# Optimization experiments

Measured on AMD Instinct MI355X. Metric: run time of the kernel, lower is better.

## Reference

```python
import jax, jax.numpy as jnp
from jax import lax
import numpy as np

B, H, W = 4, 2048, 2048
FG_DENSITY = 0.1  # below 8-connectivity percolation threshold -> small components


def setup_inputs() -> dict:
    key = jax.random.key(0)
    # binary foreground mask, as the torch module expects (x == 1 selects pixels)
    x = (jax.random.uniform(key, (B, H, W)) < FG_DENSITY).astype(jnp.float32)
    return {"x": x}


def _pool3x3(m):
    # torch.nn.MaxPool2d(kernel=3, stride=1, padding=1); -inf padding matches
    # torch's max-pool padding semantics (all labels are >= 0 anyway).
    return lax.reduce_window(m, -jnp.inf, lax.max,
                             window_dimensions=(1, 3, 3),
                             window_strides=(1, 1, 1),
                             padding=((0, 0), (1, 1), (1, 1)))


def reference(x):
    b, h, w = x.shape
    mult = h * w
    # per-pixel initial labels: mult - linear_index, reshaped to [H, W]
    weights = (jnp.float32(mult) - jnp.arange(mult, dtype=jnp.float32)).reshape(h, w)
    sel = x == 1.0                      # foreground selector (constant)
    mask0 = x * weights                 # background pixels get label 0

    # Iterate max-pool label propagation to the fixed point. The torch loop
    # stops when torch.unique count stabilizes; since the update is monotone
    # non-decreasing and bounded, that is exactly the fixed point reached here.
    def cond(state):
        _, converged = state
        return jnp.logical_not(converged)

    def body(state):
        m, _ = state
        new = jnp.where(sel, _pool3x3(m), m)
        return new, jnp.all(new == m)

    mask, _ = lax.while_loop(cond, body, (mask0, jnp.array(False)))
    return mask
```

## Files before the change

kernel.cpp:

```cpp
#include <hip/hip_runtime.h>


constexpr int W_DIM = 2048;
constexpr int H_DIM = 2048;
constexpr int MULT  = W_DIM * H_DIM;
constexpr int TILE  = 64;
constexpr int TPX   = TILE * TILE;
constexpr int BLK   = 256;
constexpr int TILES_PER_IMG = MULT / TPX;
constexpr int NB    = (H_DIM / TILE) - 1;
constexpr int WCAP  = 512;
constexpr int OVF_CAP = 65536;

__device__ __forceinline__ int find_root(const int* p, int v) {
    int q = p[v];
    while (q != v) { v = q; q = p[v]; }
    return v;
}

__device__ __forceinline__ void merge_uf(int* p, int a, int b) {
    while (true) {
        a = find_root(p, a);
        b = find_root(p, b);
        if (a == b) return;
        if (a < b) { int t = a; a = b; b = t; }
        int old = atomicMin(&p[a], b);
        if (old == a) return;
        a = old;
    }
}

template <int MODE>
__global__ __launch_bounds__(BLK) void cc_local(const float* __restrict__ x,
                                                int* __restrict__ parent,
                                                float* __restrict__ out,
                                                unsigned long long* __restrict__ bitmap,
                                                int2* __restrict__ slabs,
                                                int* __restrict__ wl_cnt,
                                                int2* __restrict__ ovf,
                                                int* __restrict__ ovf_cnt) {
    __shared__ int lp[TPX];
    __shared__ unsigned long long rowmask_sh[TILE];
    __shared__ unsigned int bc[TPX / 32];
    __shared__ int cursor;

    const int t    = threadIdx.x;
    const int wave = t >> 6;
    const int lane = t & 63;
    const int tile = blockIdx.x;
    const int img  = tile / TILES_PER_IMG;
    const int tl   = tile % TILES_PER_IMG;
    const int tr   = tl >> 5;
    const int tc   = tl & 31;
    const int origin = img * MULT + (tr * TILE) * W_DIM + tc * TILE;

    unsigned long long m[16];
    #pragma unroll
    for (int rr = 0; rr < 16; ++rr) {
        int row = wave * 16 + rr;
        float v = x[origin + row * W_DIM + lane];
        m[rr] = __ballot(v != 0.0f);
    }
    if (lane == 0) {
        #pragma unroll
        for (int rr = 0; rr < 16; ++rr) {
            rowmask_sh[wave * 16 + rr] = m[rr];
            if constexpr (MODE == 1) {
                int grow = tr * TILE + wave * 16 + rr;
                bitmap[(img * H_DIM + grow) * (W_DIM / 64) + tc] = m[rr];
            }
        }
    }
    if constexpr (MODE == 1) {
        if (t < TPX / 32) bc[t] = 0u;
        if (t == 0) cursor = 0;
    }
    #pragma unroll
    for (int j = 0; j < 4; ++j) {
        int s = t + BLK * j;
        int b = s * 4;
        reinterpret_cast<int4*>(lp)[s] = make_int4(b, b + 1, b + 2, b + 3);
    }
    __syncthreads();

    const unsigned long long mu0 = (wave > 0) ? rowmask_sh[wave * 16 - 1] : 0ULL;

    unsigned long long bits = 0ULL;
    #pragma unroll
    for (int rr = 0; rr < 16; ++rr) {
        const unsigned long long mm = m[rr];
        const unsigned long long mu = (rr == 0) ? mu0 : m[rr - 1];
        const unsigned long long lmask  = mm & (mm << 1);
        const unsigned long long bfmask = mm & mu & ~((mm << 1) & (mu << 1));
        const unsigned long long afmask = mm & (mu << 1) & ~mu & ~(mm << 1);
        const unsigned long long cfmask = mm & (mu >> 1) & ~mu;
        unsigned nib = (unsigned)((lmask  >> lane) & 1ULL)
                     | ((unsigned)((bfmask >> lane) & 1ULL) << 1)
                     | ((unsigned)((afmask >> lane) & 1ULL) << 2)
                     | ((unsigned)((cfmask >> lane) & 1ULL) << 3);
        bits |= (unsigned long long)nib << (rr * 4);
    }

    while (__any(bits != 0ULL)) {
        if (bits) {
            int idx = (int)__builtin_ctzll(bits);
            bits &= bits - 1;
            int rr = idx >> 2, ty = idx & 3;
            int p  = (wave * 16 + rr) * TILE + lane;
            int off = (ty & 2) ? ((ty & 1) ? -(TILE - 1) : -(TILE + 1))
                               : ((ty & 1) ? -TILE : -1);
            merge_uf(lp, p, p + off);
        }
    }
    __syncthreads();

    if constexpr (MODE == 1) {
        int p = -1;
        bool mark = false;
        if      (wave == 0) { if (tr > 0)  { p = lane;                      mark = (rowmask_sh[0]    >> lane) & 1ULL; } }
        else if (wave == 3) { if (tr < 31) { p = (TILE - 1) * TILE + lane;  mark = (rowmask_sh[63]   >> lane) & 1ULL; } }
        else if (wave == 1) { if (tc > 0)  { p = lane * TILE;               mark = rowmask_sh[lane] & 1ULL; } }
        else                { if (tc < 31) { p = lane * TILE + (TILE - 1);  mark = (rowmask_sh[lane] >> 63) & 1ULL; } }
        if (mark) {
            int v = find_root(lp, p);
            atomicOr(&bc[v >> 5], 1u << (v & 31));
            int rg = origin + (v >> 6) * W_DIM + (v & (TILE - 1));
            int pg = origin + (p >> 6) * W_DIM + (p & (TILE - 1));
            parent[pg] = rg;
        }
        __syncthreads();
    }

    unsigned ndbits = 0;
    #pragma unroll
    for (int j = 0; j < 4; ++j) {
        int s   = t + BLK * j;
        int row = s >> 4;
        int c4  = s & 15;
        int p0  = row * TILE + c4 * 4;
        int4 q  = reinterpret_cast<const int4*>(lp)[s];
        unsigned fgbits = (unsigned)((rowmask_sh[row] >> (c4 * 4)) & 0xFULL);
        int vr[4];
        {
            int v = q.x, p = p0;
            if ((fgbits & 1u) && v != p) { int w = lp[v]; while (w != v) { v = w; w = lp[v]; } }
            vr[0] = v;
        }
        {
            int v = q.y, p = p0 + 1;
            if ((fgbits & 2u) && v != p) { int w = lp[v]; while (w != v) { v = w; w = lp[v]; } }
            vr[1] = v;
        }
        {
            int v = q.z, p = p0 + 2;
            if ((fgbits & 4u) && v != p) { int w = lp[v]; while (w != v) { v = w; w = lp[v]; } }
            vr[2] = v;
        }
        {
            int v = q.w, p = p0 + 3;
            if ((fgbits & 8u) && v != p) { int w = lp[v]; while (w != v) { v = w; w = lp[v]; } }
            vr[3] = v;
        }

        if constexpr (MODE == 0) {
            int4 o;
            o.x = (fgbits & 1u) ? origin + (vr[0] >> 6) * W_DIM + (vr[0] & (TILE - 1)) : -1;
            o.y = (fgbits & 2u) ? origin + (vr[1] >> 6) * W_DIM + (vr[1] & (TILE - 1)) : -1;
            o.z = (fgbits & 4u) ? origin + (vr[2] >> 6) * W_DIM + (vr[2] & (TILE - 1)) : -1;
            o.w = (fgbits & 8u) ? origin + (vr[3] >> 6) * W_DIM + (vr[3] & (TILE - 1)) : -1;
            reinterpret_cast<int4*>(parent + origin + row * W_DIM)[c4] = o;
        } else {
            float4 o;
            float lab[4];
            #pragma unroll
            for (int k = 0; k < 4; ++k) {
                int v = vr[k];
                bool fg = (fgbits >> k) & 1u;
                int g = origin + (v >> 6) * W_DIM + (v & (TILE - 1));
                lab[k] = fg ? (float)(MULT - (g & (MULT - 1))) : 0.0f;
                bool nd = fg && ((bc[v >> 5] >> (v & 31)) & 1u);
                if (nd) {
                    ndbits |= 1u << (j * 4 + k);
                    if (v == p0 + k) parent[g] = g;
                }
            }
            o.x = lab[0]; o.y = lab[1]; o.z = lab[2]; o.w = lab[3];
            reinterpret_cast<float4*>(out + origin + row * W_DIM)[c4] = o;
        }
    }

    if constexpr (MODE == 1) {
        if (ndbits) {
            int cnt  = __popc(ndbits);
            int base = atomicAdd(&cursor, cnt);
            while (ndbits) {
                int b = (int)__builtin_ctz(ndbits);
                ndbits &= ndbits - 1;
                int j = b >> 2, k = b & 3;
                int s   = t + BLK * j;
                int row = s >> 4;
                int c4  = s & 15;
                int p   = row * TILE + c4 * 4 + k;
                int v   = find_root(lp, p);
                int g   = origin + (v >> 6) * W_DIM + (v & (TILE - 1));
                int pg  = origin + row * W_DIM + c4 * 4 + k;
                int off = base++;
                if (off < WCAP) slabs[tile * WCAP + off] = make_int2(pg, g);
                else {
                    int oi = atomicAdd(ovf_cnt, 1);
                    if (oi < OVF_CAP) ovf[oi] = make_int2(pg, g);
                }
            }
        }
        __syncthreads();
        if (t == 0) wl_cnt[tile] = (cursor < WCAP) ? cursor : WCAP;
    }
}

__global__ void cc_zero(int* p) { *p = 0; }

__global__ __launch_bounds__(BLK) void cc_border_bm(const unsigned long long* __restrict__ bm,
                                                    int* __restrict__ parent, int total) {
    int tid = blockIdx.x * blockDim.x + threadIdx.x;
    if (tid >= total) return;
    const int per_img = 2 * NB * W_DIM;
    int img = tid / per_img;
    int k   = tid % per_img;
    int base = img * MULT;
    const unsigned long long* b = bm + (size_t)img * H_DIM * (W_DIM / 64);
    auto FG = [&](int r, int c) -> bool {
        return (b[r * (W_DIM / 64) + (c >> 6)] >> (c & 63)) & 1ULL;
    };
    if (k < NB * W_DIM) {
        int r = TILE * (1 + k / W_DIM);
        int c = k % W_DIM;
        if (!FG(r, c)) return;
        int i  = base + r * W_DIM + c;
        int up = i - W_DIM;
        if (FG(r - 1, c))                    merge_uf(parent, i, up);
        if (c > 0         && FG(r - 1, c - 1)) merge_uf(parent, i, up - 1);
        if (c < W_DIM - 1 && FG(r - 1, c + 1)) merge_uf(parent, i, up + 1);
    } else {
        int m2 = k - NB * W_DIM;
        int c = TILE * (1 + m2 / H_DIM);
        int r = m2 % H_DIM;
        if (!FG(r, c)) return;
        int i   = base + r * W_DIM + c;
        int lft = i - 1;
        if (FG(r, c - 1))                      merge_uf(parent, i, lft);
        if (r > 0         && FG(r - 1, c - 1)) merge_uf(parent, i, lft - W_DIM);
        if (r < H_DIM - 1 && FG(r + 1, c - 1)) merge_uf(parent, i, lft + W_DIM);
    }
}

__global__ __launch_bounds__(BLK) void cc_fixup(const int2* __restrict__ slabs,
                                                const int* __restrict__ wl_cnt,
                                                const int2* __restrict__ ovf,
                                                const int* __restrict__ ovf_cnt,
                                                const int* __restrict__ parent,
                                                float* __restrict__ out, int ntiles) {
    int tid = blockIdx.x * blockDim.x + threadIdx.x;
    int slab_total = ntiles * WCAP;
    int2 e;
    if (tid < slab_total) {
        int tile = tid / WCAP, slot = tid - tile * WCAP;
        if (slot >= wl_cnt[tile]) return;
        e = slabs[tid];
    } else {
        int oi = tid - slab_total;
        int oc = *ovf_cnt; if (oc > OVF_CAP) oc = OVF_CAP;
        if (oi >= oc) return;
        e = ovf[oi];
    }
    int root = find_root(parent, e.y);
    out[e.x] = (float)(MULT - (root & (MULT - 1)));
}

__global__ __launch_bounds__(BLK) void cc_border(int* __restrict__ parent, int total) {
    int tid = blockIdx.x * blockDim.x + threadIdx.x;
    if (tid >= total) return;
    const int per_img = 2 * NB * W_DIM;
    int img = tid / per_img;
    int k   = tid % per_img;
    int base = img * MULT;
    if (k < NB * W_DIM) {
        int r = TILE * (1 + k / W_DIM);
        int c = k % W_DIM;
        int i = base + r * W_DIM + c;
        if (parent[i] < 0) return;
        int up = i - W_DIM;
        if (parent[up] >= 0)                      merge_uf(parent, i, up);
        if (c > 0         && parent[up - 1] >= 0) merge_uf(parent, i, up - 1);
        if (c < W_DIM - 1 && parent[up + 1] >= 0) merge_uf(parent, i, up + 1);
    } else {
        int m2 = k - NB * W_DIM;
        int c = TILE * (1 + m2 / H_DIM);
        int r = m2 % H_DIM;
        int i = base + r * W_DIM + c;
        if (parent[i] < 0) return;
        int lft = i - 1;
        if (parent[lft] >= 0)                            merge_uf(parent, i, lft);
        if (r > 0         && parent[lft - W_DIM] >= 0)   merge_uf(parent, i, lft - W_DIM);
        if (r < H_DIM - 1 && parent[lft + W_DIM] >= 0)   merge_uf(parent, i, lft + W_DIM);
    }
}

__global__ __launch_bounds__(BLK) void cc_write(const int* __restrict__ parent,
                                                float* __restrict__ out, int n4) {
    int i = blockIdx.x * blockDim.x + threadIdx.x;
    if (i >= n4) return;
    int4 p = reinterpret_cast<const int4*>(parent)[i];
    int a0 = (p.x >= 0) ? parent[p.x] : 0;
    int a1 = (p.y >= 0) ? parent[p.y] : 0;
    int a2 = (p.z >= 0) ? parent[p.z] : 0;
    int a3 = (p.w >= 0) ? parent[p.w] : 0;
    float4 o;
    { int v = p.x, w = a0; if (v >= 0) { while (w != v) { v = w; w = parent[v]; } }
      o.x = (p.x < 0) ? 0.f : (float)(MULT - (v & (MULT - 1))); }
    { int v = p.y, w = a1; if (v >= 0) { while (w != v) { v = w; w = parent[v]; } }
      o.y = (p.y < 0) ? 0.f : (float)(MULT - (v & (MULT - 1))); }
    { int v = p.z, w = a2; if (v >= 0) { while (w != v) { v = w; w = parent[v]; } }
      o.z = (p.z < 0) ? 0.f : (float)(MULT - (v & (MULT - 1))); }
    { int v = p.w, w = a3; if (v >= 0) { while (w != v) { v = w; w = parent[v]; } }
      o.w = (p.w < 0) ? 0.f : (float)(MULT - (v & (MULT - 1))); }
    reinterpret_cast<float4*>(out)[i] = o;
}

__global__ __launch_bounds__(BLK) void cc_flatten(int* __restrict__ parent, int n) {
    int i = blockIdx.x * blockDim.x + threadIdx.x;
    if (i >= n) return;
    int p = parent[i];
    if (p < 0 || p == i) return;
    int r = find_root(parent, p);
    if (r != p) parent[i] = r;
}

__global__ __launch_bounds__(BLK) void cc_final_inplace(int* __restrict__ parent, int n4) {
    int i = blockIdx.x * blockDim.x + threadIdx.x;
    if (i >= n4) return;
    int4 p = reinterpret_cast<const int4*>(parent)[i];
    float4 o;
    o.x = (p.x < 0) ? 0.f : (float)(MULT - (p.x & (MULT - 1)));
    o.y = (p.y < 0) ? 0.f : (float)(MULT - (p.y & (MULT - 1)));
    o.z = (p.z < 0) ? 0.f : (float)(MULT - (p.z & (MULT - 1)));
    o.w = (p.w < 0) ? 0.f : (float)(MULT - (p.w & (MULT - 1)));
    reinterpret_cast<float4*>(parent)[i] = o;
}

extern "C" void kernel_launch(void* const* d_in, const int* in_sizes, int n_in,
                              void* d_out, int out_size, void* d_ws, size_t ws_size,
                              hipStream_t stream) {
    const float* x = (const float*)d_in[0];
    const int n     = in_sizes[0];
    const int n_img = n / MULT;
    const int n4    = n / 4;
    const int tiles = n_img * TILES_PER_IMG;
    const int border_threads = n_img * 2 * NB * W_DIM;

    size_t off_parent = 0;
    size_t off_bitmap = off_parent + (size_t)n * 4;
    size_t off_slabs  = off_bitmap + (size_t)n / 8;
    size_t off_cnt    = off_slabs  + (size_t)tiles * WCAP * 8;
    size_t off_ovf    = off_cnt    + (size_t)tiles * 4;
    size_t off_ovfcnt = off_ovf    + (size_t)OVF_CAP * 8;
    size_t need_fused = off_ovfcnt + 128;

    dim3 blk(BLK);
    if (ws_size >= need_fused) {
        char* ws = (char*)d_ws;
        int*  parent  = (int*)(ws + off_parent);
        unsigned long long* bitmap = (unsigned long long*)(ws + off_bitmap);
        int2* slabs   = (int2*)(ws + off_slabs);
        int*  wl_cnt  = (int*)(ws + off_cnt);
        int2* ovf     = (int2*)(ws + off_ovf);
        int*  ovf_cnt = (int*)(ws + off_ovfcnt);
        float* out    = (float*)d_out;

        cc_zero<<<1, 1, 0, stream>>>(ovf_cnt);
        cc_local<1><<<tiles, blk, 0, stream>>>(x, parent, out, bitmap,
                                               slabs, wl_cnt, ovf, ovf_cnt);
        cc_border_bm<<<(border_threads + BLK - 1) / BLK, blk, 0, stream>>>(bitmap, parent, border_threads);
        int fix_threads = tiles * WCAP + OVF_CAP;
        cc_fixup<<<(fix_threads + BLK - 1) / BLK, blk, 0, stream>>>(slabs, wl_cnt, ovf, ovf_cnt,
                                                                    parent, out, tiles);
    } else {
        const bool use_ws = (ws_size >= (size_t)n * sizeof(int));
        int* parent = use_ws ? (int*)d_ws : (int*)d_out;
        cc_local<0><<<tiles, blk, 0, stream>>>(x, parent, nullptr, nullptr,
                                               nullptr, nullptr, nullptr, nullptr);
        cc_border<<<(border_threads + BLK - 1) / BLK, blk, 0, stream>>>(parent, border_threads);
        if (use_ws) {
            cc_write<<<(n4 + BLK - 1) / BLK, blk, 0, stream>>>(parent, (float*)d_out, n4);
        } else {
            cc_flatten      <<<(n + BLK - 1) / BLK, blk, 0, stream>>>(parent, n);
            cc_final_inplace<<<(n4 + BLK - 1) / BLK, blk, 0, stream>>>(parent, n4);
        }
    }
}
```

Measured before the change: 64.04 us.

## Pack border-root flag into local parent array and enqueue worklist inline

Stores the 'touches tile border' flag as a high bit in the shared union-find parent array instead of a separate bitmap, so the final root walk yields both root and flag. Worklist entries are appended inline with per-element shared atomics instead of a second find_root pass. Root self-parent writes move to the border-marking step. The fixup kernel skips writes when the root did not change, and the zeroing kernel is replaced by a memset. The trade-off is more contended shared-memory atomics on the cursor and an extra mask in every find step.

```diff
diff --git a/kernel.cpp b/kernel.cpp
--- a/kernel.cpp
+++ b/kernel.cpp
@@ -11,10 +11,18 @@
 constexpr int NB    = (H_DIM / TILE) - 1;
 constexpr int WCAP  = 512;
 constexpr int OVF_CAP = 65536;
+constexpr int PMASK = 0xFFFF;
+constexpr int BFLAG = 0x10000;
 
 __device__ __forceinline__ int find_root(const int* p, int v) {
     int q = p[v];
     while (q != v) { v = q; q = p[v]; }
+    return v;
+}
+
+__device__ __forceinline__ int find_root_m(const int* p, int v) {
+    int q = p[v] & PMASK;
+    while (q != v) { v = q; q = p[v] & PMASK; }
     return v;
 }
 
@@ -41,7 +49,6 @@
                                                 int* __restrict__ ovf_cnt) {
     __shared__ int lp[TPX];
     __shared__ unsigned long long rowmask_sh[TILE];
-    __shared__ unsigned int bc[TPX / 32];
     __shared__ int cursor;
 
     const int t    = threadIdx.x;
@@ -52,7 +59,9 @@
     const int tl   = tile % TILES_PER_IMG;
     const int tr   = tl >> 5;
     const int tc   = tl & 31;
-    const int origin = img * MULT + (tr * TILE) * W_DIM + tc * TILE;
+    const int origin    = img * MULT + (tr * TILE) * W_DIM + tc * TILE;
+    const int img_base  = img * MULT;
+    const int base_loc  = origin - img_base;
 
     unsigned long long m[16];
     #pragma unroll
@@ -72,7 +81,6 @@
         }
     }
     if constexpr (MODE == 1) {
-        if (t < TPX / 32) bc[t] = 0u;
         if (t == 0) cursor = 0;
     }
     #pragma unroll
@@ -122,44 +130,60 @@
         else if (wave == 1) { if (tc > 0)  { p = lane * TILE;               mark = rowmask_sh[lane] & 1ULL; } }
         else                { if (tc < 31) { p = lane * TILE + (TILE - 1);  mark = (rowmask_sh[lane] >> 63) & 1ULL; } }
         if (mark) {
-            int v = find_root(lp, p);
-            atomicOr(&bc[v >> 5], 1u << (v & 31));
+            int v = find_root_m(lp, p);
+            atomicOr(&lp[v], BFLAG);
             int rg = origin + (v >> 6) * W_DIM + (v & (TILE - 1));
             int pg = origin + (p >> 6) * W_DIM + (p & (TILE - 1));
             parent[pg] = rg;
+            parent[rg] = rg;
         }
         __syncthreads();
     }
 
-    unsigned ndbits = 0;
     #pragma unroll
     for (int j = 0; j < 4; ++j) {
         int s   = t + BLK * j;
         int row = s >> 4;
         int c4  = s & 15;
         int p0  = row * TILE + c4 * 4;
-        int4 q  = reinterpret_cast<const int4*>(lp)[s];
+        int4 qv = reinterpret_cast<const int4*>(lp)[s];
         unsigned fgbits = (unsigned)((rowmask_sh[row] >> (c4 * 4)) & 0xFULL);
-        int vr[4];
+        int vr[4], qf[4];
         {
-            int v = q.x, p = p0;
-            if ((fgbits & 1u) && v != p) { int w = lp[v]; while (w != v) { v = w; w = lp[v]; } }
-            vr[0] = v;
+            int q = qv.x, v = q & PMASK, p = p0;
+            if ((fgbits & 1u) && v != p) {
+                int w = lp[v];
+                while ((w & PMASK) != v) { v = w & PMASK; w = lp[v]; }
+                q = w;
+            }
+            vr[0] = v; qf[0] = q;
         }
         {
-            int v = q.y, p = p0 + 1;
-            if ((fgbits & 2u) && v != p) { int w = lp[v]; while (w != v) { v = w; w = lp[v]; } }
-            vr[1] = v;
+            int q = qv.y, v = q & PMASK, p = p0 + 1;
+            if ((fgbits & 2u) && v != p) {
+                int w = lp[v];
+                while ((w & PMASK) != v) { v = w & PMASK; w = lp[v]; }
+                q = w;
+            }
+            vr[1] = v; qf[1] = q;
         }
         {
-            int v = q.z, p = p0 + 2;
-            if ((fgbits & 4u) && v != p) { int w = lp[v]; while (w != v) { v = w; w = lp[v]; } }
-            vr[2] = v;
+            int q = qv.z, v = q & PMASK, p = p0 + 2;
+            if ((fgbits & 4u) && v != p) {
+                int w = lp[v];
+                while ((w & PMASK) != v) { v = w & PMASK; w = lp[v]; }
+                q = w;
+            }
+            vr[2] = v; qf[2] = q;
         }
         {
-            int v = q.w, p = p0 + 3;
-            if ((fgbits & 8u) && v != p) { int w = lp[v]; while (w != v) { v = w; w = lp[v]; } }
-            vr[3] = v;
+            int q = qv.w, v = q & PMASK, p = p0 + 3;
+            if ((fgbits & 8u) && v != p) {
+                int w = lp[v];
+                while ((w & PMASK) != v) { v = w & PMASK; w = lp[v]; }
+                q = w;
+            }
+            vr[3] = v; qf[3] = q;
         }
 
         if constexpr (MODE == 0) {
@@ -170,54 +194,34 @@
             o.w = (fgbits & 8u) ? origin + (vr[3] >> 6) * W_DIM + (vr[3] & (TILE - 1)) : -1;
             reinterpret_cast<int4*>(parent + origin + row * W_DIM)[c4] = o;
         } else {
-            float4 o;
             float lab[4];
             #pragma unroll
             for (int k = 0; k < 4; ++k) {
-                int v = vr[k];
+                int v  = vr[k];
                 bool fg = (fgbits >> k) & 1u;
-                int g = origin + (v >> 6) * W_DIM + (v & (TILE - 1));
-                lab[k] = fg ? (float)(MULT - (g & (MULT - 1))) : 0.0f;
-                bool nd = fg && ((bc[v >> 5] >> (v & 31)) & 1u);
-                if (nd) {
-                    ndbits |= 1u << (j * 4 + k);
-                    if (v == p0 + k) parent[g] = g;
+                int rl = base_loc + ((v >> 6) << 11) + (v & (TILE - 1));
+                lab[k] = fg ? (float)(MULT - rl) : 0.0f;
+                if (fg && (qf[k] & BFLAG)) {
+                    int off = atomicAdd(&cursor, 1);
+                    int pg  = origin + row * W_DIM + c4 * 4 + k;
+                    int g   = img_base + rl;
+                    if (off < WCAP) slabs[tile * WCAP + off] = make_int2(pg, g);
+                    else {
+                        int oi = atomicAdd(ovf_cnt, 1);
+                        if (oi < OVF_CAP) ovf[oi] = make_int2(pg, g);
+                    }
                 }
             }
-            o.x = lab[0]; o.y = lab[1]; o.z = lab[2]; o.w = lab[3];
+            float4 o; o.x = lab[0]; o.y = lab[1]; o.z = lab[2]; o.w = lab[3];
             reinterpret_cast<float4*>(out + origin + row * W_DIM)[c4] = o;
         }
     }
 
     if constexpr (MODE == 1) {
-        if (ndbits) {
-            int cnt  = __popc(ndbits);
-            int base = atomicAdd(&cursor, cnt);
-            while (ndbits) {
-                int b = (int)__builtin_ctz(ndbits);
-                ndbits &= ndbits - 1;
-                int j = b >> 2, k = b & 3;
-                int s   = t + BLK * j;
-                int row = s >> 4;
-                int c4  = s & 15;
-                int p   = row * TILE + c4 * 4 + k;
-                int v   = find_root(lp, p);
-                int g   = origin + (v >> 6) * W_DIM + (v & (TILE - 1));
-                int pg  = origin + row * W_DIM + c4 * 4 + k;
-                int off = base++;
-                if (off < WCAP) slabs[tile * WCAP + off] = make_int2(pg, g);
-                else {
-                    int oi = atomicAdd(ovf_cnt, 1);
-                    if (oi < OVF_CAP) ovf[oi] = make_int2(pg, g);
-                }
-            }
-        }
         __syncthreads();
         if (t == 0) wl_cnt[tile] = (cursor < WCAP) ? cursor : WCAP;
     }
 }
-
-__global__ void cc_zero(int* p) { *p = 0; }
 
 __global__ __launch_bounds__(BLK) void cc_border_bm(const unsigned long long* __restrict__ bm,
                                                     int* __restrict__ parent, int total) {
@@ -237,7 +241,7 @@
         if (!FG(r, c)) return;
         int i  = base + r * W_DIM + c;
         int up = i - W_DIM;
-        if (FG(r - 1, c))                    merge_uf(parent, i, up);
+        if (FG(r - 1, c))                      merge_uf(parent, i, up);
         if (c > 0         && FG(r - 1, c - 1)) merge_uf(parent, i, up - 1);
         if (c < W_DIM - 1 && FG(r - 1, c + 1)) merge_uf(parent, i, up + 1);
     } else {
@@ -273,7 +277,7 @@
         e = ovf[oi];
     }
     int root = find_root(parent, e.y);
-    out[e.x] = (float)(MULT - (root & (MULT - 1)));
+    if (root != e.y) out[e.x] = (float)(MULT - (root & (MULT - 1)));
 }
 
 __global__ __launch_bounds__(BLK) void cc_border(int* __restrict__ parent, int total) {
@@ -376,7 +380,7 @@
         int*  ovf_cnt = (int*)(ws + off_ovfcnt);
         float* out    = (float*)d_out;
 
-        cc_zero<<<1, 1, 0, stream>>>(ovf_cnt);
+        hipMemsetAsync(ovf_cnt, 0, sizeof(int), stream);
         cc_local<1><<<tiles, blk, 0, stream>>>(x, parent, out, bitmap,
                                                slabs, wl_cnt, ovf, ovf_cnt);
         cc_border_bm<<<(border_threads + BLK - 1) / BLK, blk, 0, stream>>>(bitmap, parent, border_threads);
```

After: 60.43 us. 5.6% less time.
